# Performance work log

Hardware: AMD Instinct MI355X
Metric: run time of the kernel (lower is better)

## Reference

```python
import jax, jax.numpy as jnp
import numpy as np

N, D_IN, D_OUT, H, E = 8192, 1024, 1024, 1024, 8
EPS = 0.2
S_FACTOR = 5.0


def setup_inputs() -> dict:
    key = jax.random.key(0)
    k0, k1, k2, k3 = jax.random.split(key, 4)
    x = jax.random.normal(k0, (N, D_IN), jnp.float32)
    # selector Linear(nIn, E); weights scaled by sFactor as in SMoE.__init__
    Wsel = jax.random.normal(k1, (D_IN, E), jnp.float32) * (S_FACTOR / np.sqrt(D_IN))
    bsel = jnp.zeros((E,), jnp.float32)
    # stacked 2-layer MLP experts: Linear(D_IN,H) -> ReLU -> Linear(H,D_OUT)
    W1 = jax.random.normal(k2, (E, D_IN, H), jnp.float32) / np.sqrt(D_IN)
    b1 = jnp.zeros((E, H), jnp.float32)
    W2 = jax.random.normal(k3, (E, H, D_OUT), jnp.float32) / np.sqrt(H)
    b2 = jnp.zeros((E, D_OUT), jnp.float32)
    return {"x": x, "Wsel": Wsel, "bsel": bsel, "W1": W1, "b1": b1, "W2": W2, "b2": b2}


def _sparse_weights(weightMat):
    # sort experts per token, descending (torch.sort(..., 1, descending=True))
    order = jnp.argsort(-weightMat, axis=1)                # [N,E]
    topW = jnp.take_along_axis(weightMat, order, axis=1)
    cumW = jnp.cumsum(topW, axis=1)
    capped = jnp.minimum(cumW, 1.0 - EPS)
    sw_sorted = jax.nn.relu(capped - cumW + topW)          # sparse weights, sorted order
    # softCost (side-effect metric in the original; not returned by SMoE.forward)
    shifted = jnp.pad(sw_sorted[:, 1:], ((0, 0), (0, 1)))
    _soft_cost = jnp.sum(jnp.where(shifted > 0, 1.0, sw_sorted), axis=1)
    # faithful to torch.gather(sparse_weight, 1, index) in the source
    sw = jnp.take_along_axis(sw_sorted, order, axis=1)     # [N,E]
    return sw


def reference(x, Wsel, bsel, W1, b1, W2, b2):
    weightMat = jax.nn.softmax(x @ Wsel + bsel, axis=1)    # [N,E] selector
    sw = _sparse_weights(weightMat)                        # [N,E] sparse combine weights
    # dense (vectorized) expert dispatch: tokens with sw==0 contribute 0,
    # numerically identical to the gather/scatter_add loop in sparse_MoE
    h = jax.nn.relu(jnp.einsum('nd,edh->enh', x, W1) + b1[:, None, :])   # [E,N,H]
    y = jnp.einsum('enh,eho->eno', h, W2) + b2[:, None, :]               # [E,N,O]
    out = jnp.einsum('ne,eno->no', sw, y)                                # [N,O]
    return out
```

## Files before the change

### kernel.cpp

```cpp
#include <hip/hip_runtime.h>
#include <hip/hip_bf16.h>
#include <stdint.h>

#define N_TOK 8192
#define DIN   1024
#define DOUT  1024
#define HID   1024
#define NE    8
#define CAP   0.8f

typedef __attribute__((ext_vector_type(8))) short short8;
typedef __attribute__((ext_vector_type(4))) float floatx4;

__device__ __forceinline__ void async_load16(const void* g, void* l) {
  __builtin_amdgcn_global_load_lds(
      (const __attribute__((address_space(1))) void*)g,
      (__attribute__((address_space(3))) void*)l,
      16, 0, 0);
}

__device__ __forceinline__ unsigned short bf16_bits(float f) {
  return __builtin_bit_cast(unsigned short, __float2bfloat16(f));
}

__global__ __launch_bounds__(256) void zero_kernel(float4* __restrict__ out4, int n4) {
  const int stride = gridDim.x * 256;
  for (int i = blockIdx.x * 256 + threadIdx.x; i < n4; i += stride)
    out4[i] = (float4){0.f, 0.f, 0.f, 0.f};
}

__global__ __launch_bounds__(256) void selector_kernel(
    const float* __restrict__ x, const float* __restrict__ Wsel,
    const float* __restrict__ bsel,
    __hip_bfloat16* __restrict__ x_bf, float* __restrict__ sw)
{
  const int lane = threadIdx.x & 63;
  const int wave = threadIdx.x >> 6;
  const int n = blockIdx.x * 4 + wave;
  const float4* xr4 = (const float4*)(x + (size_t)n * DIN);
  ushort4* xb4 = (ushort4*)(x_bf + (size_t)n * DIN);

  float acc[8];
#pragma unroll
  for (int e = 0; e < 8; e++) acc[e] = 0.f;

#pragma unroll
  for (int i = 0; i < 4; i++) {
    const int d4 = lane + i * 64;
    const float4 xv = xr4[d4];
    ushort4 p;
    p.x = bf16_bits(xv.x);
    p.y = bf16_bits(xv.y);
    p.z = bf16_bits(xv.z);
    p.w = bf16_bits(xv.w);
    xb4[d4] = p;
    const float xs[4] = {xv.x, xv.y, xv.z, xv.w};
#pragma unroll
    for (int q = 0; q < 4; q++) {
      const int d = d4 * 4 + q;
      const float4* wr = (const float4*)(Wsel + d * 8);
      const float4 wlo = wr[0], whi = wr[1];
      const float xv1 = xs[q];
      acc[0] += xv1 * wlo.x; acc[1] += xv1 * wlo.y;
      acc[2] += xv1 * wlo.z; acc[3] += xv1 * wlo.w;
      acc[4] += xv1 * whi.x; acc[5] += xv1 * whi.y;
      acc[6] += xv1 * whi.z; acc[7] += xv1 * whi.w;
    }
  }
#pragma unroll
  for (int off = 32; off >= 1; off >>= 1)
#pragma unroll
    for (int e = 0; e < 8; e++) acc[e] += __shfl_xor(acc[e], off);

  if (lane == 0) {
    float w[8];
    float mx = -1e30f;
#pragma unroll
    for (int e = 0; e < 8; e++) { w[e] = acc[e] + bsel[e]; mx = fmaxf(mx, w[e]); }
    float s = 0.f;
#pragma unroll
    for (int e = 0; e < 8; e++) { w[e] = expf(w[e] - mx); s += w[e]; }
    const float inv = 1.f / s;
#pragma unroll
    for (int e = 0; e < 8; e++) w[e] *= inv;

    float wsrt[8]; int ord[8];
    for (int k = 0; k < 8; k++) {
      const float v = w[k];
      int j = k;
      while (j > 0 && wsrt[j - 1] < v) { wsrt[j] = wsrt[j - 1]; ord[j] = ord[j - 1]; j--; }
      wsrt[j] = v; ord[j] = k;
    }
    float cum = 0.f, sws[8];
    for (int k = 0; k < 8; k++) {
      cum += wsrt[k];
      const float capped = fminf(cum, CAP);
      sws[k] = fmaxf(capped - cum + wsrt[k], 0.f);
    }
    for (int j = 0; j < 8; j++) sw[(size_t)n * 8 + j] = sws[ord[j]];
  }
}

__global__ __launch_bounds__(1024) void compact_kernel(
    const float* __restrict__ sw, int* __restrict__ idx, int* __restrict__ cnt)
{
  const int e = blockIdx.x;
  const int t = threadIdx.x;
  const int lane = t & 63;
  const int wv = t >> 6;
  __shared__ int wave_base[16];
  __shared__ int chunk_total;
  int base = 0;
#pragma unroll
  for (int c = 0; c < 8; c++) {
    const int tok = c * 1024 + t;
    const bool act = sw[(size_t)tok * 8 + e] > 0.f;
    const unsigned long long m = __ballot(act);
    const int before = __popcll(m & ((1ull << lane) - 1ull));
    if (lane == 0) wave_base[wv] = __popcll(m);
    __syncthreads();
    if (t == 0) {
      int s = 0;
      for (int w = 0; w < 16; w++) { const int v = wave_base[w]; wave_base[w] = s; s += v; }
      chunk_total = s;
    }
    __syncthreads();
    if (act) idx[e * N_TOK + base + wave_base[wv] + before] = tok;
    base += chunk_total;
    __syncthreads();
  }
  if (t == 0) cnt[e] = base;
}

__global__ __launch_bounds__(256) void convert_weights_kernel(
    const float* __restrict__ W1, const float* __restrict__ W2,
    __hip_bfloat16* __restrict__ W1t, __hip_bfloat16* __restrict__ W2t)
{
  __shared__ float tile[32][33];
  const int z = blockIdx.z;
  const float* src = (z & 8) ? W2 : W1;
  __hip_bfloat16* dst = (z & 8) ? W2t : W1t;
  const int e = z & 7;
  src += (size_t)e * 1024 * 1024;
  dst += (size_t)e * 1024 * 1024;
  const int R = blockIdx.y * 32, C = blockIdx.x * 32;
  const int c = threadIdx.x & 31, r0 = threadIdx.x >> 5;
#pragma unroll
  for (int p = 0; p < 4; p++) {
    const int r = r0 + p * 8;
    tile[r][c] = src[(size_t)(R + r) * 1024 + C + c];
  }
  __syncthreads();
#pragma unroll
  for (int p = 0; p < 4; p++) {
    const int r = r0 + p * 8;
    dst[(size_t)(C + r) * 1024 + R + c] = __float2bfloat16(tile[c][r]);
  }
}

template <int MODE>
__global__ __launch_bounds__(256, 3) void moe_gemm(
    const __hip_bfloat16* __restrict__ x_bf,
    __hip_bfloat16* __restrict__ hpool,
    const __hip_bfloat16* __restrict__ Wt,
    const float* __restrict__ biasAll,
    const float* __restrict__ sw,
    const int* __restrict__ idx, const int* __restrict__ cnt,
    float* __restrict__ out)
{
  const int id = blockIdx.x;
  const int n = id & 7;
  const int q = id >> 3;
  const int mslot = q & 63;
  const int e = q >> 6;

  const int count = cnt[e];
  const int m0 = mslot * 128;
  if (m0 >= count) return;
  const int n0 = n * 128;

  __shared__ __align__(16) __hip_bfloat16 sA[128 * 64];
  __shared__ __align__(16) __hip_bfloat16 sB[128 * 64];
  const int t = threadIdx.x;
  const int lane = t & 63;
  const int wave = t >> 6;
  const int wm = (wave & 1) * 64;
  const int wn = (wave >> 1) * 64;
  const int* idx_e = idx + e * N_TOK;
  const float* bias = biasAll + e * 1024;

  floatx4 acc[4][4];
#pragma unroll
  for (int i = 0; i < 4; i++)
#pragma unroll
    for (int j = 0; j < 4; j++) acc[i][j] = (floatx4){0.f, 0.f, 0.f, 0.f};

  const int r0 = t >> 3;
  const int c8 = t & 7;
  const int g8 = ((c8 + r0) & 7) * 8;
  const __hip_bfloat16* Arow[4];
#pragma unroll
  for (int p = 0; p < 4; p++) {
    if (MODE == 0) {
      const int tok = idx_e[min(m0 + r0 + p * 32, count - 1)];
      Arow[p] = x_bf + (size_t)tok * 1024;
    } else {
      Arow[p] = hpool + ((size_t)e * N_TOK + m0 + r0 + p * 32) * 1024;
    }
  }
  const __hip_bfloat16* Brow = Wt + (size_t)e * 1024 * 1024 + (size_t)(n0 + r0) * 1024;
  __hip_bfloat16* lA = &sA[r0 * 64 + c8 * 8];
  __hip_bfloat16* lB = &sB[r0 * 64 + c8 * 8];

  const int rf = lane & 15;
  const int gquad = lane >> 4;

  for (int k0 = 0; k0 < 1024; k0 += 64) {
#pragma unroll
    for (int p = 0; p < 4; p++) {
      async_load16(Arow[p] + k0 + g8, lA + p * 32 * 64);
      async_load16(Brow + (size_t)p * 32 * 1024 + k0 + g8, lB + p * 32 * 64);
    }
    __syncthreads();
#pragma unroll
    for (int kk = 0; kk < 2; kk++) {
      const int gc = gquad + kk * 4;
      short8 aF[4], bF[4];
#pragma unroll
      for (int i = 0; i < 4; i++) {
        const int r = wm + i * 16 + rf;
        aF[i] = *(const short8*)&sA[r * 64 + ((gc - r) & 7) * 8];
      }
#pragma unroll
      for (int j = 0; j < 4; j++) {
        const int r = wn + j * 16 + rf;
        bF[j] = *(const short8*)&sB[r * 64 + ((gc - r) & 7) * 8];
      }
#pragma unroll
      for (int i = 0; i < 4; i++)
#pragma unroll
        for (int j = 0; j < 4; j++)
          acc[i][j] = __builtin_amdgcn_mfma_f32_16x16x32_bf16(aF[i], bF[j], acc[i][j], 0, 0, 0);
    }
    __syncthreads();
  }

  const int quad = lane >> 4;
  const int cn = lane & 15;
#pragma unroll
  for (int i = 0; i < 4; i++) {
#pragma unroll
    for (int r = 0; r < 4; r++) {
      const int gm = m0 + wm + i * 16 + quad * 4 + r;
      if (gm >= count) continue;
      int tok = 0; float swv = 0.f;
      if (MODE == 1) {
        tok = idx_e[gm];
        swv = sw[tok * 8 + e];
      }
#pragma unroll
      for (int j = 0; j < 4; j++) {
        const int gn = n0 + wn + j * 16 + cn;
        const float v = acc[i][j][r] + bias[gn];
        if (MODE == 0) {
          hpool[((size_t)e * N_TOK + gm) * 1024 + gn] = __float2bfloat16(fmaxf(v, 0.f));
        } else {
          unsafeAtomicAdd(&out[(size_t)tok * 1024 + gn], swv * v);
        }
      }
    }
  }
}

extern "C" void kernel_launch(void* const* d_in, const int* in_sizes, int n_in,
                              void* d_out, int out_size, void* d_ws, size_t ws_size,
                              hipStream_t stream) {
  const float* x    = (const float*)d_in[0];
  const float* Wsel = (const float*)d_in[1];
  const float* bsel = (const float*)d_in[2];
  const float* W1   = (const float*)d_in[3];
  const float* b1   = (const float*)d_in[4];
  const float* W2   = (const float*)d_in[5];
  const float* b2   = (const float*)d_in[6];
  float* out = (float*)d_out;

  char* ws = (char*)d_ws;
  __hip_bfloat16* x_bf = (__hip_bfloat16*)ws; ws += (size_t)N_TOK * DIN * 2;
  __hip_bfloat16* W1t  = (__hip_bfloat16*)ws; ws += (size_t)NE * DIN * HID * 2;
  __hip_bfloat16* W2t  = (__hip_bfloat16*)ws; ws += (size_t)NE * HID * DOUT * 2;
  float* sw            = (float*)ws;          ws += (size_t)N_TOK * NE * 4;
  int* idx             = (int*)ws;            ws += (size_t)NE * N_TOK * 4;
  int* cnt             = (int*)ws;            ws += 256;
  __hip_bfloat16* hpool = (__hip_bfloat16*)ws;

  zero_kernel<<<1024, 256, 0, stream>>>((float4*)out, N_TOK * DOUT / 4);
  selector_kernel<<<N_TOK / 4, 256, 0, stream>>>(x, Wsel, bsel, x_bf, sw);
  compact_kernel<<<NE, 1024, 0, stream>>>(sw, idx, cnt);
  convert_weights_kernel<<<dim3(32, 32, 16), 256, 0, stream>>>(W1, W2, W1t, W2t);

  moe_gemm<0><<<8 * 64 * 8, 256, 0, stream>>>(
      x_bf, hpool, W1t, b1, sw, idx, cnt, out);
  moe_gemm<1><<<8 * 64 * 8, 256, 0, stream>>>(
      x_bf, hpool, W2t, b2, sw, idx, cnt, out);
}
```

Measured before the change: 332.1 us.

## Replace atomic scatter-add with bf16 expert output pool and gather combine

The second expert GEMM now writes its outputs in bf16 to a per-expert pool, and the compact kernel records each token's slot in every expert's compacted list. A new combine kernel then gathers each token's active expert rows and writes the weighted sum directly. This removes the output zeroing pass and the fp32 atomic adds to the output. In exchange it adds an intermediate buffer write and read, rounds expert outputs to bf16, and falls back to the atomic path when the workspace is too small.

```diff
diff --git a/kernel.cpp b/kernel.cpp
--- a/kernel.cpp
+++ b/kernel.cpp
@@ -21,6 +21,9 @@
 
 __device__ __forceinline__ unsigned short bf16_bits(float f) {
   return __builtin_bit_cast(unsigned short, __float2bfloat16(f));
+}
+__device__ __forceinline__ float bits_to_f32(unsigned short b) {
+  return __builtin_bit_cast(float, (unsigned int)b << 16);
 }
 
 __global__ __launch_bounds__(256) void zero_kernel(float4* __restrict__ out4, int n4) {
@@ -102,7 +105,8 @@
 }
 
 __global__ __launch_bounds__(1024) void compact_kernel(
-    const float* __restrict__ sw, int* __restrict__ idx, int* __restrict__ cnt)
+    const float* __restrict__ sw, int* __restrict__ idx,
+    int* __restrict__ pos, int* __restrict__ cnt)
 {
   const int e = blockIdx.x;
   const int t = threadIdx.x;
@@ -125,7 +129,11 @@
       chunk_total = s;
     }
     __syncthreads();
-    if (act) idx[e * N_TOK + base + wave_base[wv] + before] = tok;
+    if (act) {
+      const int p = base + wave_base[wv] + before;
+      idx[e * N_TOK + p] = tok;
+      pos[(size_t)tok * 8 + e] = p;
+    }
     base += chunk_total;
     __syncthreads();
   }
@@ -162,6 +170,7 @@
 __global__ __launch_bounds__(256, 3) void moe_gemm(
     const __hip_bfloat16* __restrict__ x_bf,
     __hip_bfloat16* __restrict__ hpool,
+    __hip_bfloat16* __restrict__ ypool,
     const __hip_bfloat16* __restrict__ Wt,
     const float* __restrict__ biasAll,
     const float* __restrict__ sw,
@@ -254,7 +263,7 @@
       const int gm = m0 + wm + i * 16 + quad * 4 + r;
       if (gm >= count) continue;
       int tok = 0; float swv = 0.f;
-      if (MODE == 1) {
+      if (MODE == 2) {
         tok = idx_e[gm];
         swv = sw[tok * 8 + e];
       }
@@ -264,11 +273,55 @@
         const float v = acc[i][j][r] + bias[gn];
         if (MODE == 0) {
           hpool[((size_t)e * N_TOK + gm) * 1024 + gn] = __float2bfloat16(fmaxf(v, 0.f));
+        } else if (MODE == 1) {
+          ypool[((size_t)e * N_TOK + gm) * 1024 + gn] = __float2bfloat16(v);
         } else {
           unsafeAtomicAdd(&out[(size_t)tok * 1024 + gn], swv * v);
         }
       }
     }
+  }
+}
+
+__global__ __launch_bounds__(256) void combine_kernel(
+    const float* __restrict__ sw, const int* __restrict__ pos,
+    const __hip_bfloat16* __restrict__ ypool, float* __restrict__ out)
+{
+  const int lane = threadIdx.x & 63;
+  const int wave = threadIdx.x >> 6;
+  const int n = blockIdx.x * 4 + wave;
+
+  const float4* swr = (const float4*)(sw + (size_t)n * 8);
+  const float4 s0 = swr[0], s1 = swr[1];
+  const float swl[8] = {s0.x, s0.y, s0.z, s0.w, s1.x, s1.y, s1.z, s1.w};
+  const int4* pr = (const int4*)(pos + (size_t)n * 8);
+  const int4 p0 = pr[0], p1 = pr[1];
+  const int pl[8] = {p0.x, p0.y, p0.z, p0.w, p1.x, p1.y, p1.z, p1.w};
+
+  float acc[16];
+#pragma unroll
+  for (int i = 0; i < 16; i++) acc[i] = 0.f;
+
+#pragma unroll
+  for (int j = 0; j < 8; j++) {
+    if (swl[j] > 0.f) {
+      const float wj = swl[j];
+      const unsigned short* yr =
+          (const unsigned short*)(ypool + ((size_t)j * N_TOK + pl[j]) * 1024);
+#pragma unroll
+      for (int q = 0; q < 4; q++) {
+        const ushort4 v = *(const ushort4*)(yr + q * 256 + lane * 4);
+        acc[q * 4 + 0] += wj * bits_to_f32(v.x);
+        acc[q * 4 + 1] += wj * bits_to_f32(v.y);
+        acc[q * 4 + 2] += wj * bits_to_f32(v.z);
+        acc[q * 4 + 3] += wj * bits_to_f32(v.w);
+      }
+    }
+  }
+#pragma unroll
+  for (int q = 0; q < 4; q++) {
+    float4 o = {acc[q * 4 + 0], acc[q * 4 + 1], acc[q * 4 + 2], acc[q * 4 + 3]};
+    *(float4*)(out + (size_t)n * 1024 + q * 256 + lane * 4) = o;
   }
 }
 
@@ -290,16 +343,26 @@
   __hip_bfloat16* W2t  = (__hip_bfloat16*)ws; ws += (size_t)NE * HID * DOUT * 2;
   float* sw            = (float*)ws;          ws += (size_t)N_TOK * NE * 4;
   int* idx             = (int*)ws;            ws += (size_t)NE * N_TOK * 4;
+  int* pos             = (int*)ws;            ws += (size_t)NE * N_TOK * 4;
   int* cnt             = (int*)ws;            ws += 256;
-  __hip_bfloat16* hpool = (__hip_bfloat16*)ws;
-
-  zero_kernel<<<1024, 256, 0, stream>>>((float4*)out, N_TOK * DOUT / 4);
+  __hip_bfloat16* hpool = (__hip_bfloat16*)ws; ws += (size_t)NE * N_TOK * HID * 2;
+  __hip_bfloat16* ypool = (__hip_bfloat16*)ws;
+  const size_t need_pool = (size_t)(ws - (char*)d_ws) + (size_t)NE * N_TOK * DOUT * 2;
+  const bool pooled = ws_size >= need_pool;
+
   selector_kernel<<<N_TOK / 4, 256, 0, stream>>>(x, Wsel, bsel, x_bf, sw);
-  compact_kernel<<<NE, 1024, 0, stream>>>(sw, idx, cnt);
+  compact_kernel<<<NE, 1024, 0, stream>>>(sw, idx, pos, cnt);
   convert_weights_kernel<<<dim3(32, 32, 16), 256, 0, stream>>>(W1, W2, W1t, W2t);
 
   moe_gemm<0><<<8 * 64 * 8, 256, 0, stream>>>(
-      x_bf, hpool, W1t, b1, sw, idx, cnt, out);
-  moe_gemm<1><<<8 * 64 * 8, 256, 0, stream>>>(
-      x_bf, hpool, W2t, b2, sw, idx, cnt, out);
-}
+      x_bf, hpool, ypool, W1t, b1, sw, idx, cnt, out);
+  if (pooled) {
+    moe_gemm<1><<<8 * 64 * 8, 256, 0, stream>>>(
+        x_bf, hpool, ypool, W2t, b2, sw, idx, cnt, out);
+    combine_kernel<<<N_TOK / 4, 256, 0, stream>>>(sw, pos, ypool, out);
+  } else {
+    zero_kernel<<<1024, 256, 0, stream>>>((float4*)out, N_TOK * DOUT / 4);
+    moe_gemm<2><<<8 * 64 * 8, 256, 0, stream>>>(
+        x_bf, hpool, ypool, W2t, b2, sw, idx, cnt, out);
+  }
+}
```

New measurement: 335.7 us. Within noise of the previous version (+1.1%).
